# Kernel optimization log

Hardware: AMD Instinct MI355X
Metric: run time of the kernel (lower is better)

The kernel has to match this reference:

```python
import jax, jax.numpy as jnp
import numpy as np

DIM = 512
HEADS = 8
HEAD_DIM = DIM // HEADS
MLP_HIDDEN = int(DIM * 4.0)
B, N = 4, 2048
LS_INIT = 1e-5
EPS = 1e-5


def _layernorm(x, w, b):
    mu = jnp.mean(x, axis=-1, keepdims=True)
    var = jnp.mean(jnp.square(x - mu), axis=-1, keepdims=True)
    return (x - mu) * jax.lax.rsqrt(var + EPS) * w + b


def setup_inputs() -> dict:
    key = jax.random.key(0)
    ks = jax.random.split(key, 12)
    s = 0.02
    return {
        "x": jax.random.normal(ks[0], (B, N, DIM), jnp.float32),
        "rel_pos_bias": jax.random.normal(ks[1], (HEADS, N, N), jnp.float32),
        "qkv_w": jax.random.normal(ks[2], (DIM, 3 * DIM), jnp.float32) * s,
        "qkv_b": jnp.zeros((3 * DIM,), jnp.float32),
        "out_w": jax.random.normal(ks[3], (DIM, DIM), jnp.float32) * s,
        "out_b": jnp.zeros((DIM,), jnp.float32),
        "ln1_w": jnp.ones((DIM,), jnp.float32),
        "ln1_b": jnp.zeros((DIM,), jnp.float32),
        "ln2_w": jnp.ones((DIM,), jnp.float32),
        "ln2_b": jnp.zeros((DIM,), jnp.float32),
        "ffn_w1": jax.random.normal(ks[4], (DIM, MLP_HIDDEN), jnp.float32) * s,
        "ffn_b1": jnp.zeros((MLP_HIDDEN,), jnp.float32),
        "ffn_w2": jax.random.normal(ks[5], (MLP_HIDDEN, DIM), jnp.float32) * s,
        "ffn_b2": jnp.zeros((DIM,), jnp.float32),
        "gamma1": jnp.full((DIM,), LS_INIT, jnp.float32),
        "gamma2": jnp.full((DIM,), LS_INIT, jnp.float32),
    }


def reference(x, rel_pos_bias, qkv_w, qkv_b, out_w, out_b, ln1_w, ln1_b,
              ln2_w, ln2_b, ffn_w1, ffn_b1, ffn_w2, ffn_b2, gamma1, gamma2):
    # Pre-norm MHA with relative-position bias
    y = _layernorm(x, ln1_w, ln1_b)                       # [B,N,C]
    qkv = y @ qkv_w + qkv_b                               # [B,N,3C]
    qkv = qkv.reshape(B, N, 3, HEADS, HEAD_DIM)
    q = jnp.transpose(qkv[:, :, 0], (0, 2, 1, 3))         # [B,H,N,D]
    k = jnp.transpose(qkv[:, :, 1], (0, 2, 1, 3))
    v = jnp.transpose(qkv[:, :, 2], (0, 2, 1, 3))
    scale = 1.0 / np.sqrt(HEAD_DIM).astype(np.float32)
    attn = jnp.einsum("bhid,bhjd->bhij", q, k) * scale    # [B,H,N,N]
    attn = attn + rel_pos_bias[None]
    attn = jax.nn.softmax(attn, axis=-1)
    out = jnp.einsum("bhij,bhjd->bhid", attn, v)          # [B,H,N,D]
    out = jnp.transpose(out, (0, 2, 1, 3)).reshape(B, N, DIM)
    out = out @ out_w + out_b
    x = x + out * gamma1                                  # layer scale, no drop-path (eval)
    # FFN with exact GELU
    y2 = _layernorm(x, ln2_w, ln2_b)
    h = jax.nn.gelu(y2 @ ffn_w1 + ffn_b1, approximate=False)
    ffn_out = h @ ffn_w2 + ffn_b2
    x = x + ffn_out * gamma2
    return x
```

## Files before the change

kernel.cpp:

```cpp
#include <hip/hip_runtime.h>
#include <hip/hip_bf16.h>
#include <math.h>

#define SEQ 2048
#define BATCH 4
#define DM 512
#define NH 8
#define HD 64
#define HID 2048
#define ROWS (BATCH * SEQ)

typedef __attribute__((ext_vector_type(8))) short short8;
typedef __attribute__((ext_vector_type(4))) float f32x4;

__device__ __forceinline__ short f2bf(float f) {
    unsigned u = __float_as_uint(f);
    u += 0x7fff + ((u >> 16) & 1);
    return (short)(u >> 16);
}

__device__ __forceinline__ void gl2lds16(const void* g, void* l) {
    __builtin_amdgcn_global_load_lds(
        (const __attribute__((address_space(1))) void*)g,
        (__attribute__((address_space(3))) void*)l, 16, 0, 0);
}

__global__ __launch_bounds__(256) void tcast_all(
    const float* __restrict__ qkv_w, const float* __restrict__ out_w,
    const float* __restrict__ w1, const float* __restrict__ w2,
    short* __restrict__ o_qkv, short* __restrict__ o_out,
    short* __restrict__ o_w1, short* __restrict__ o_w2) {
    __shared__ float tile[32][33];
    int id = blockIdx.x;
    const float* W; short* O; int K, N;
    if (id < 768)       { W = qkv_w; O = o_qkv; K = 512;  N = 1536; }
    else if (id < 1024) { W = out_w; O = o_out; K = 512;  N = 512;  id -= 768; }
    else if (id < 2048) { W = w1;    O = o_w1;  K = 512;  N = 2048; id -= 1024; }
    else                { W = w2;    O = o_w2;  K = 2048; N = 512;  id -= 2048; }
    int tn = N / 32;
    int n0 = (id % tn) * 32, k0 = (id / tn) * 32;
    int tx = threadIdx.x, ty = threadIdx.y;
#pragma unroll
    for (int i = 0; i < 4; ++i)
        tile[ty + i * 8][tx] = W[(size_t)(k0 + ty + i * 8) * N + n0 + tx];
    __syncthreads();
#pragma unroll
    for (int i = 0; i < 4; ++i)
        O[(size_t)(n0 + ty + i * 8) * K + k0 + tx] = f2bf(tile[tx][ty + i * 8]);
}

__global__ __launch_bounds__(256) void ln_k(const float* __restrict__ X,
                                            const float* __restrict__ g,
                                            const float* __restrict__ bta,
                                            short* __restrict__ Y) {
    int t = threadIdx.x;
    int wv = t >> 6, ln = t & 63;
    size_t row = (size_t)blockIdx.x * 4 + wv;
    const float* xr = X + row * DM;
    float4 v0 = *(const float4*)(xr + ln * 4);
    float4 v1 = *(const float4*)(xr + 256 + ln * 4);
    float s = v0.x + v0.y + v0.z + v0.w + v1.x + v1.y + v1.z + v1.w;
    float q = v0.x * v0.x + v0.y * v0.y + v0.z * v0.z + v0.w * v0.w +
              v1.x * v1.x + v1.y * v1.y + v1.z * v1.z + v1.w * v1.w;
#pragma unroll
    for (int off = 1; off < 64; off <<= 1) {
        s += __shfl_xor(s, off);
        q += __shfl_xor(q, off);
    }
    float mean = s * (1.0f / 512.0f);
    float var = q * (1.0f / 512.0f) - mean * mean;
    float rstd = rsqrtf(var + 1e-5f);
    int c0 = ln * 4, c1 = 256 + ln * 4;
    ushort4 o0, o1;
    o0.x = (unsigned short)f2bf((v0.x - mean) * rstd * g[c0 + 0] + bta[c0 + 0]);
    o0.y = (unsigned short)f2bf((v0.y - mean) * rstd * g[c0 + 1] + bta[c0 + 1]);
    o0.z = (unsigned short)f2bf((v0.z - mean) * rstd * g[c0 + 2] + bta[c0 + 2]);
    o0.w = (unsigned short)f2bf((v0.w - mean) * rstd * g[c0 + 3] + bta[c0 + 3]);
    o1.x = (unsigned short)f2bf((v1.x - mean) * rstd * g[c1 + 0] + bta[c1 + 0]);
    o1.y = (unsigned short)f2bf((v1.y - mean) * rstd * g[c1 + 1] + bta[c1 + 1]);
    o1.z = (unsigned short)f2bf((v1.z - mean) * rstd * g[c1 + 2] + bta[c1 + 2]);
    o1.w = (unsigned short)f2bf((v1.w - mean) * rstd * g[c1 + 3] + bta[c1 + 3]);
    *(ushort4*)((unsigned short*)Y + row * DM + c0) = o0;
    *(ushort4*)((unsigned short*)Y + row * DM + c1) = o1;
}

template <int EPI, int TN, int BM>
__global__ __launch_bounds__(256) void gemm_bt(const short* __restrict__ A,
                                               const short* __restrict__ Bt,
                                               const float* __restrict__ bias,
                                               const float* __restrict__ gamma,
                                               const float* __restrict__ res,
                                               void* __restrict__ Cout,
                                               int M, int N, int K, int gx) {
    constexpr int NI = TN / 32;
    constexpr int MI = BM / 32;
    __shared__ __attribute__((aligned(16))) short As[2][2][BM][32];
    __shared__ __attribute__((aligned(16))) short Bs[2][2][TN][32];
    int t = threadIdx.x;
    int w = t >> 6, ln = t & 63;
    int quad = ln >> 4, l15 = ln & 15;
    int nwg = gridDim.x;
    int qq = nwg >> 3;
    int sw = ((blockIdx.x & 7) * qq) + (blockIdx.x >> 3);
    int bx = sw % gx, by = sw / gx;
    int n0 = bx * TN, m0 = by * BM;
    int wm = (w & 1) * (BM / 2), wn = (w >> 1) * (TN / 2);

    int srow0 = w * 32 + (ln >> 2);
    int srow1 = srow0 + 16;
    int srowH = w * 16 + (ln >> 2);
    int schunk = (ln & 3) * 8;
    const short* Ag0 = A + (size_t)(m0 + srow0) * K + schunk;
    const short* Ag1 = A + (size_t)(m0 + srow1) * K + schunk;
    const short* AgH = A + (size_t)(m0 + srowH) * K + schunk;
    const short* Bg0 = Bt + (size_t)(n0 + srow0) * K + schunk;
    const short* Bg1 = Bt + (size_t)(n0 + srow1) * K + schunk;
    const short* BgH = Bt + (size_t)(n0 + srowH) * K + schunk;

    f32x4 acc[MI][NI];
#pragma unroll
    for (int i = 0; i < MI; ++i)
#pragma unroll
        for (int j = 0; j < NI; ++j) acc[i][j] = (f32x4){0.f, 0.f, 0.f, 0.f};

    auto STAGE = [&](int buf, int k0) {
        if constexpr (BM == 128) {
            gl2lds16(Ag0 + k0, &As[buf][0][srow0][schunk]);
            gl2lds16(Ag1 + k0, &As[buf][0][srow1][schunk]);
            gl2lds16(Ag0 + k0 + 32, &As[buf][1][srow0][schunk]);
            gl2lds16(Ag1 + k0 + 32, &As[buf][1][srow1][schunk]);
        } else {
            gl2lds16(AgH + k0, &As[buf][0][srowH][schunk]);
            gl2lds16(AgH + k0 + 32, &As[buf][1][srowH][schunk]);
        }
        if constexpr (TN == 128) {
            gl2lds16(Bg0 + k0, &Bs[buf][0][srow0 & 127][schunk]);
            gl2lds16(Bg1 + k0, &Bs[buf][0][srow1 & 127][schunk]);
            gl2lds16(Bg0 + k0 + 32, &Bs[buf][1][srow0 & 127][schunk]);
            gl2lds16(Bg1 + k0 + 32, &Bs[buf][1][srow1 & 127][schunk]);
        } else {
            gl2lds16(BgH + k0, &Bs[buf][0][srowH & (TN - 1)][schunk]);
            gl2lds16(BgH + k0 + 32, &Bs[buf][1][srowH & (TN - 1)][schunk]);
        }
    };

    STAGE(0, 0);
    __syncthreads();

    int NS = K >> 6;
    for (int s = 0; s < NS; ++s) {
        int cur = s & 1;
        if (s + 1 < NS) STAGE(cur ^ 1, (s + 1) << 6);
#pragma unroll
        for (int hh = 0; hh < 2; ++hh) {
            short8 af[MI], bf[NI];
#pragma unroll
            for (int mi = 0; mi < MI; ++mi)
                af[mi] = *(const short8*)&As[cur][hh][wm + mi * 16 + l15][quad * 8];
#pragma unroll
            for (int ni = 0; ni < NI; ++ni)
                bf[ni] = *(const short8*)&Bs[cur][hh][wn + ni * 16 + l15][quad * 8];
#pragma unroll
            for (int mi = 0; mi < MI; ++mi)
#pragma unroll
                for (int ni = 0; ni < NI; ++ni)
                    acc[mi][ni] = __builtin_amdgcn_mfma_f32_16x16x32_bf16(
                        af[mi], bf[ni], acc[mi][ni], 0, 0, 0);
        }
        __syncthreads();
    }

#pragma unroll
    for (int mi = 0; mi < MI; ++mi) {
#pragma unroll
        for (int ni = 0; ni < NI; ++ni) {
#pragma unroll
            for (int r = 0; r < 4; ++r) {
                int row = m0 + wm + mi * 16 + quad * 4 + r;
                int col = n0 + wn + ni * 16 + l15;
                float v = acc[mi][ni][r] + bias[col];
                if (EPI == 0) {
                    ((short*)Cout)[(size_t)row * N + col] = f2bf(v);
                } else if (EPI == 1) {
                    float u = v * fmaf(v * v, 0.0713548162f, 1.59576912f);
                    float gg = v / (1.0f + __expf(-u));
                    ((short*)Cout)[(size_t)row * N + col] = f2bf(gg);
                } else {
                    ((float*)Cout)[(size_t)row * N + col] =
                        fmaf(v, gamma[col], res[(size_t)row * N + col]);
                }
            }
        }
    }
}

__global__ __launch_bounds__(256) void qkvbias_k(
    const short* __restrict__ A, const short* __restrict__ Bt,
    const float* __restrict__ qkvb, short* __restrict__ Cout,
    short* __restrict__ Cout2,
    const float* __restrict__ bias, short* __restrict__ biasP) {
    __shared__ __attribute__((aligned(16))) char smem[33024];
    int bid = blockIdx.x;
    int grp = bid / 11, sub = bid % 11;
    int t = threadIdx.x;
    int w = t >> 6, ln = t & 63;
    int quad = ln >> 4, l15 = ln & 15;

    if (sub < 3) {
        typedef short (*tile32)[32];
        tile32 As0 = (tile32)smem;
        tile32 As1 = (tile32)(smem + 8192);
        tile32 Bs0 = (tile32)(smem + 16384);
        tile32 Bs1 = (tile32)(smem + 24576);
        const int K = 512, N = 1536;
        int g = grp * 3 + sub;
        int n0 = (g % 12) * 128, m0 = (g / 12) * 128;
        int wm = (w & 1) * 64, wn = (w >> 1) * 64;

        int srow0 = w * 32 + (ln >> 2);
        int srow1 = srow0 + 16;
        int schunk = (ln & 3) * 8;
        const short* Ag0 = A + (size_t)(m0 + srow0) * K + schunk;
        const short* Ag1 = A + (size_t)(m0 + srow1) * K + schunk;
        const short* Bg0 = Bt + (size_t)(n0 + srow0) * K + schunk;
        const short* Bg1 = Bt + (size_t)(n0 + srow1) * K + schunk;

        f32x4 acc[4][4];
#pragma unroll
        for (int i = 0; i < 4; ++i)
#pragma unroll
            for (int j = 0; j < 4; ++j) acc[i][j] = (f32x4){0.f, 0.f, 0.f, 0.f};

        for (int k0 = 0; k0 < K; k0 += 64) {
            __syncthreads();
            gl2lds16(Ag0 + k0, &As0[srow0][schunk]);
            gl2lds16(Ag1 + k0, &As0[srow1][schunk]);
            gl2lds16(Ag0 + k0 + 32, &As1[srow0][schunk]);
            gl2lds16(Ag1 + k0 + 32, &As1[srow1][schunk]);
            gl2lds16(Bg0 + k0, &Bs0[srow0][schunk]);
            gl2lds16(Bg1 + k0, &Bs0[srow1][schunk]);
            gl2lds16(Bg0 + k0 + 32, &Bs1[srow0][schunk]);
            gl2lds16(Bg1 + k0 + 32, &Bs1[srow1][schunk]);
            __syncthreads();
            {
                short8 af[4], bf[4];
#pragma unroll
                for (int mi = 0; mi < 4; ++mi)
                    af[mi] = *(const short8*)&As0[wm + mi * 16 + l15][quad * 8];
#pragma unroll
                for (int ni = 0; ni < 4; ++ni)
                    bf[ni] = *(const short8*)&Bs0[wn + ni * 16 + l15][quad * 8];
#pragma unroll
                for (int mi = 0; mi < 4; ++mi)
#pragma unroll
                    for (int ni = 0; ni < 4; ++ni)
                        acc[mi][ni] = __builtin_amdgcn_mfma_f32_16x16x32_bf16(
                            af[mi], bf[ni], acc[mi][ni], 0, 0, 0);
            }
            {
                short8 af[4], bf[4];
#pragma unroll
                for (int mi = 0; mi < 4; ++mi)
                    af[mi] = *(const short8*)&As1[wm + mi * 16 + l15][quad * 8];
#pragma unroll
                for (int ni = 0; ni < 4; ++ni)
                    bf[ni] = *(const short8*)&Bs1[wn + ni * 16 + l15][quad * 8];
#pragma unroll
                for (int mi = 0; mi < 4; ++mi)
#pragma unroll
                    for (int ni = 0; ni < 4; ++ni)
                        acc[mi][ni] = __builtin_amdgcn_mfma_f32_16x16x32_bf16(
                            af[mi], bf[ni], acc[mi][ni], 0, 0, 0);
            }
        }

        if (n0 >= 1024) {
#pragma unroll
            for (int mi = 0; mi < 4; ++mi) {
#pragma unroll
                for (int ni = 0; ni < 4; ++ni) {
                    int col = n0 + wn + ni * 16 + l15;
                    int d = col - 1024, hh = d >> 6, dd = d & 63;
                    int row0 = m0 + wm + mi * 16 + quad * 4;
                    int bb = row0 >> 11, key = row0 & 2047;
                    float bs = qkvb[col];
                    ushort4 pk;
                    pk.x = (unsigned short)f2bf(acc[mi][ni][0] + bs);
                    pk.y = (unsigned short)f2bf(acc[mi][ni][1] + bs);
                    pk.z = (unsigned short)f2bf(acc[mi][ni][2] + bs);
                    pk.w = (unsigned short)f2bf(acc[mi][ni][3] + bs);
                    *(ushort4*)&Cout2[((size_t)(bb * 8 + hh) * 64 + dd) * 2048 + key] = pk;
                }
            }
        } else {
#pragma unroll
            for (int mi = 0; mi < 4; ++mi) {
#pragma unroll
                for (int ni = 0; ni < 4; ++ni) {
#pragma unroll
                    for (int r = 0; r < 4; ++r) {
                        int row = m0 + wm + mi * 16 + quad * 4 + r;
                        int col = n0 + wn + ni * 16 + l15;
                        float v = acc[mi][ni][r] + qkvb[col];
                        float sc = (n0 < 512) ? 0.18033688f : 1.0f;
                        Cout[(size_t)row * 1024 + col] = f2bf(v * sc);
                    }
                }
            }
        }
    } else {
        typedef short (*tile1032)[1032];
        tile1032 tl = (tile1032)smem;
        int id = grp * 8 + (sub - 3);
        int half = id & 1;
        int g = (id >> 1) & 127;
        int h = id >> 8;
        const float* src = bias + (size_t)h * SEQ * SEQ + (size_t)g * 16 * SEQ + half * 1024;
#pragma unroll
        for (int i = 0; i < 16; ++i) {
            float4 v = *(const float4*)(src + (size_t)i * SEQ + t * 4);
            float2 lo, hi;
            lo.x = v.x * 1.44269504f; lo.y = v.y * 1.44269504f;
            hi.x = v.z * 1.44269504f; hi.y = v.w * 1.44269504f;
            __hip_bfloat162 l2 = __float22bfloat162_rn(lo);
            __hip_bfloat162 h2 = __float22bfloat162_rn(hi);
            uint2 pp;
            pp.x = *(unsigned*)&l2;
            pp.y = *(unsigned*)&h2;
            *(uint2*)&tl[i][t * 4] = pp;
        }
        __syncthreads();
        int jtbase = half * 16;
#pragma unroll
        for (int u = 0; u < 4; ++u) {
            int jl = w * 4 + u;
            int tau = (h * 128 + g) * 32 + jtbase + jl;
#pragma unroll
            for (int n2 = 0; n2 < 2; ++n2) {
                uint2 a = *(const uint2*)&tl[l15][jl * 64 + n2 * 32 + quad * 4];
                uint2 b = *(const uint2*)&tl[l15][jl * 64 + n2 * 32 + 16 + quad * 4];
                uint4 pp;
                pp.x = a.x; pp.y = a.y; pp.z = b.x; pp.w = b.y;
                *(uint4*)(biasP + (size_t)tau * 1024 + n2 * 512 + ln * 8) = pp;
            }
        }
    }
}

__global__ __launch_bounds__(256, 3) void attn_k(const short* __restrict__ qkv,
                                                 const short* __restrict__ vT,
                                                 const short* __restrict__ biasP,
                                                 short* __restrict__ Aout) {
    __shared__ __attribute__((aligned(16))) short Ks[2][64 * 64];
    __shared__ __attribute__((aligned(16))) short Vs[2][64 * 64];
    __shared__ __attribute__((aligned(16))) short Ps[4][2][16 * 64];
    int t = threadIdx.x;
    int w = t >> 6, ln = t & 63, quad = ln >> 4, l15 = ln & 15;
    int idx = blockIdx.x;
    int h = idx & 7, b = (idx >> 3) & 3, qt = idx >> 5;
    int qb = qt * 128 + w * 16;
    const size_t cbase = (size_t)b * SEQ * 1024;

    const short* qrow0 = qkv + cbase + (size_t)(qb + l15) * 1024 + h * 64;
    const short* qrow1 = qrow0 + (size_t)64 * 1024;
    short8 qf[2][2];
    qf[0][0] = *(const short8*)(qrow0 + quad * 8);
    qf[0][1] = *(const short8*)(qrow0 + 32 + quad * 8);
    qf[1][0] = *(const short8*)(qrow1 + quad * 8);
    qf[1][1] = *(const short8*)(qrow1 + 32 + quad * 8);

    int kr = t >> 3, kc = t & 7;
    int sc = (kc ^ (kr & 7)) * 8;
    const short* kgS = qkv + cbase + 512 + h * 64 + sc;
    const short* vgS = vT + (size_t)(b * 8 + h) * 64 * 2048 + sc;

    int g0 = qt * 8 + w;
    const short* bp0 = biasP + ((size_t)(h * 128 + g0) * 32) * 1024 + ln * 8;
    const short* bp1 = biasP + ((size_t)(h * 128 + g0 + 4) * 32) * 1024 + ln * 8;

    short8 ones;
#pragma unroll
    for (int i = 0; i < 8; ++i) ones[i] = (short)0x3F80;

    f32x4 o[2][4], ol[2];
#pragma unroll
    for (int qg = 0; qg < 2; ++qg) {
#pragma unroll
        for (int db = 0; db < 4; ++db) o[qg][db] = (f32x4){0.f, 0.f, 0.f, 0.f};
        ol[qg] = (f32x4){0.f, 0.f, 0.f, 0.f};
    }

    int sw7 = l15 & 7;

    gl2lds16(kgS,                              &Ks[0][t * 8]);
    gl2lds16(kgS + (size_t)32 * 1024,          &Ks[0][2048 + t * 8]);
    gl2lds16(vgS,                              &Vs[0][t * 8]);
    gl2lds16(vgS + (size_t)32 * 2048,          &Vs[0][2048 + t * 8]);
    uint4 bbc[2][2];
#pragma unroll
    for (int n2 = 0; n2 < 2; ++n2) {
        bbc[0][n2] = *(const uint4*)(bp0 + n2 * 512);
        bbc[1][n2] = *(const uint4*)(bp1 + n2 * 512);
    }

    int cur = 0;
    for (int jt = 0; jt < 32; ++jt) {
        __syncthreads();
        int jn = (jt < 31) ? (jt + 1) : jt;
        int j1 = jn * 64;
        int nxt = cur ^ 1;
        gl2lds16(kgS + (size_t)(j1 + kr) * 1024,      &Ks[nxt][t * 8]);
        gl2lds16(kgS + (size_t)(j1 + 32 + kr) * 1024, &Ks[nxt][2048 + t * 8]);
        gl2lds16(vgS + (size_t)kr * 2048 + j1,        &Vs[nxt][t * 8]);
        gl2lds16(vgS + (size_t)(32 + kr) * 2048 + j1, &Vs[nxt][2048 + t * 8]);

        f32x4 s4[2][4];
#pragma unroll
        for (int ni = 0; ni < 4; ++ni) {
            short8 k0 = *(const short8*)&Ks[cur][(ni * 16 + l15) * 64 + ((quad ^ sw7) * 8)];
            short8 k1 = *(const short8*)&Ks[cur][(ni * 16 + l15) * 64 + (((4 + quad) ^ sw7) * 8)];
#pragma unroll
            for (int qg = 0; qg < 2; ++qg) {
                uint4 bb = bbc[qg][ni >> 1];
                unsigned lo = (ni & 1) ? bb.z : bb.x;
                unsigned hi = (ni & 1) ? bb.w : bb.y;
                f32x4 z;
                z[0] = __uint_as_float(lo << 16);
                z[1] = __uint_as_float(lo & 0xffff0000u);
                z[2] = __uint_as_float(hi << 16);
                z[3] = __uint_as_float(hi & 0xffff0000u);
                z = __builtin_amdgcn_mfma_f32_16x16x32_bf16(k0, qf[qg][0], z, 0, 0, 0);
                s4[qg][ni] = __builtin_amdgcn_mfma_f32_16x16x32_bf16(k1, qf[qg][1], z, 0, 0, 0);
            }
        }
#pragma unroll
        for (int n2 = 0; n2 < 2; ++n2) {
            bbc[0][n2] = *(const uint4*)(bp0 + (size_t)jn * 1024 + n2 * 512);
            bbc[1][n2] = *(const uint4*)(bp1 + (size_t)jn * 1024 + n2 * 512);
        }
#pragma unroll
        for (int qg = 0; qg < 2; ++qg) {
#pragma unroll
            for (int ni = 0; ni < 4; ++ni) {
                float2 plo, phi;
                plo.x = exp2f(s4[qg][ni][0]);
                plo.y = exp2f(s4[qg][ni][1]);
                phi.x = exp2f(s4[qg][ni][2]);
                phi.y = exp2f(s4[qg][ni][3]);
                __hip_bfloat162 l2 = __float22bfloat162_rn(plo);
                __hip_bfloat162 h2 = __float22bfloat162_rn(phi);
                union { uint2 u; } pp;
                pp.u.x = *(unsigned*)&l2;
                pp.u.y = *(unsigned*)&h2;
                int c = ni * 2 + (quad >> 1);
                *(uint2*)&Ps[w][qg][l15 * 64 + ((c ^ sw7) * 8) + (quad & 1) * 4] = pp.u;
            }
        }
#pragma unroll
        for (int kk = 0; kk < 2; ++kk) {
            short8 ap0 = *(const short8*)&Ps[w][0][l15 * 64 + (((kk * 4 + quad) ^ sw7) * 8)];
            short8 ap1 = *(const short8*)&Ps[w][1][l15 * 64 + (((kk * 4 + quad) ^ sw7) * 8)];
#pragma unroll
            for (int db = 0; db < 4; ++db) {
                short8 vv = *(const short8*)&Vs[cur][(db * 16 + l15) * 64 + (((kk * 4 + quad) ^ sw7) * 8)];
                o[0][db] = __builtin_amdgcn_mfma_f32_16x16x32_bf16(ap0, vv, o[0][db], 0, 0, 0);
                o[1][db] = __builtin_amdgcn_mfma_f32_16x16x32_bf16(ap1, vv, o[1][db], 0, 0, 0);
            }
            ol[0] = __builtin_amdgcn_mfma_f32_16x16x32_bf16(ap0, ones, ol[0], 0, 0, 0);
            ol[1] = __builtin_amdgcn_mfma_f32_16x16x32_bf16(ap1, ones, ol[1], 0, 0, 0);
        }
        cur = nxt;
    }
#pragma unroll
    for (int qg = 0; qg < 2; ++qg) {
#pragma unroll
        for (int r = 0; r < 4; ++r) {
            float inv = 1.0f / ol[qg][r];
            int qrow_g = b * SEQ + qb + qg * 64 + quad * 4 + r;
#pragma unroll
            for (int db = 0; db < 4; ++db) {
                Aout[(size_t)qrow_g * DM + h * 64 + db * 16 + l15] =
                    f2bf(o[qg][db][r] * inv);
            }
        }
    }
}

extern "C" void kernel_launch(void* const* d_in, const int* in_sizes, int n_in,
                              void* d_out, int out_size, void* d_ws, size_t ws_size,
                              hipStream_t stream) {
    const float* x      = (const float*)d_in[0];
    const float* bias   = (const float*)d_in[1];
    const float* qkv_w  = (const float*)d_in[2];
    const float* qkv_b  = (const float*)d_in[3];
    const float* out_w  = (const float*)d_in[4];
    const float* out_b  = (const float*)d_in[5];
    const float* ln1_w  = (const float*)d_in[6];
    const float* ln1_b  = (const float*)d_in[7];
    const float* ln2_w  = (const float*)d_in[8];
    const float* ln2_b  = (const float*)d_in[9];
    const float* ffn_w1 = (const float*)d_in[10];
    const float* ffn_b1 = (const float*)d_in[11];
    const float* ffn_w2 = (const float*)d_in[12];
    const float* ffn_b2 = (const float*)d_in[13];
    const float* gamma1 = (const float*)d_in[14];
    const float* gamma2 = (const float*)d_in[15];
    float* out = (float*)d_out;

    short* wqkvT = (short*)d_ws;
    short* woutT = wqkvT + (size_t)1536 * 512;
    short* w1T   = woutT + (size_t)512 * 512;
    short* w2T   = w1T + (size_t)2048 * 512;
    short* y1    = w2T + (size_t)512 * 2048;
    short* qkvB  = y1 + (size_t)ROWS * DM;
    short* vTb   = qkvB + (size_t)ROWS * 1024;
    short* aoutB = vTb + (size_t)32 * 64 * 2048;
    float* x1    = (float*)(aoutB + (size_t)ROWS * DM);
    short* biasPw = (short*)(x1 + (size_t)ROWS * DM);
    short* hB    = qkvB;

    tcast_all<<<3072, dim3(32, 8), 0, stream>>>(qkv_w, out_w, ffn_w1, ffn_w2,
                                                wqkvT, woutT, w1T, w2T);
    ln_k<<<ROWS / 4, 256, 0, stream>>>(x, ln1_w, ln1_b, y1);
    qkvbias_k<<<2816, 256, 0, stream>>>(y1, wqkvT, qkv_b, qkvB, vTb,
                                        bias, biasPw);
    attn_k<<<512, 256, 0, stream>>>(qkvB, vTb, biasPw, aoutB);
    gemm_bt<2, 128, 64><<<512, 256, 0, stream>>>(
        aoutB, woutT, out_b, gamma1, x, x1, ROWS, 512, 512, 4);
    ln_k<<<ROWS / 4, 256, 0, stream>>>(x1, ln2_w, ln2_b, y1);
    gemm_bt<1, 128, 128><<<1024, 256, 0, stream>>>(
        y1, w1T, ffn_b1, nullptr, nullptr, hB, ROWS, 2048, 512, 16);
    gemm_bt<2, 128, 64><<<512, 256, 0, stream>>>(
        hB, w2T, ffn_b2, gamma2, x1, out, ROWS, 512, 2048, 4);
}
```

Baseline: 420.7 us.

## Merge weight cast, LN1 and bias repack into one prep kernel; standalone QKV GEMM

Weight transpose-cast, the first layernorm and the rel-pos-bias repack now run as interleaved block roles inside a single prep kernel. The QKV GEMM moves out of the bias-repack kernel into the templated double-buffered gemm_bt with a new epilogue that scales q and writes V transposed. The aim is to overlap the memory-bound prep work across all CUs, cut one launch, and let the QKV GEMM use the pipelined GEMM path. In exchange, the QKV GEMM no longer overlaps with the bias repack.

```diff
diff --git a/kernel.cpp b/kernel.cpp
--- a/kernel.cpp
+++ b/kernel.cpp
@@ -25,28 +25,105 @@
         (__attribute__((address_space(3))) void*)l, 16, 0, 0);
 }
 
-__global__ __launch_bounds__(256) void tcast_all(
+__global__ __launch_bounds__(256) void prep_k(
     const float* __restrict__ qkv_w, const float* __restrict__ out_w,
     const float* __restrict__ w1, const float* __restrict__ w2,
     short* __restrict__ o_qkv, short* __restrict__ o_out,
-    short* __restrict__ o_w1, short* __restrict__ o_w2) {
-    __shared__ float tile[32][33];
-    int id = blockIdx.x;
-    const float* W; short* O; int K, N;
-    if (id < 768)       { W = qkv_w; O = o_qkv; K = 512;  N = 1536; }
-    else if (id < 1024) { W = out_w; O = o_out; K = 512;  N = 512;  id -= 768; }
-    else if (id < 2048) { W = w1;    O = o_w1;  K = 512;  N = 2048; id -= 1024; }
-    else                { W = w2;    O = o_w2;  K = 2048; N = 512;  id -= 2048; }
-    int tn = N / 32;
-    int n0 = (id % tn) * 32, k0 = (id / tn) * 32;
-    int tx = threadIdx.x, ty = threadIdx.y;
-#pragma unroll
-    for (int i = 0; i < 4; ++i)
-        tile[ty + i * 8][tx] = W[(size_t)(k0 + ty + i * 8) * N + n0 + tx];
-    __syncthreads();
-#pragma unroll
-    for (int i = 0; i < 4; ++i)
-        O[(size_t)(n0 + ty + i * 8) * K + k0 + tx] = f2bf(tile[tx][ty + i * 8]);
+    short* __restrict__ o_w1, short* __restrict__ o_w2,
+    const float* __restrict__ X, const float* __restrict__ lg,
+    const float* __restrict__ lb, short* __restrict__ Y,
+    const float* __restrict__ bias, short* __restrict__ biasP) {
+    __shared__ __attribute__((aligned(16))) char smem[33024];
+    int bid = blockIdx.x;
+    int grp = bid / 7, sub = bid % 7;
+    int t = threadIdx.x;
+
+    if (sub < 3) {
+        float (*tile)[33] = (float(*)[33])smem;
+        int id = grp * 3 + sub;
+        const float* W; short* O; int K, N;
+        if (id < 768)       { W = qkv_w; O = o_qkv; K = 512;  N = 1536; }
+        else if (id < 1024) { W = out_w; O = o_out; K = 512;  N = 512;  id -= 768; }
+        else if (id < 2048) { W = w1;    O = o_w1;  K = 512;  N = 2048; id -= 1024; }
+        else                { W = w2;    O = o_w2;  K = 2048; N = 512;  id -= 2048; }
+        int tn = N / 32;
+        int n0 = (id % tn) * 32, k0 = (id / tn) * 32;
+        int tx = t & 31, ty = t >> 5;
+#pragma unroll
+        for (int i = 0; i < 4; ++i)
+            tile[ty + i * 8][tx] = W[(size_t)(k0 + ty + i * 8) * N + n0 + tx];
+        __syncthreads();
+#pragma unroll
+        for (int i = 0; i < 4; ++i)
+            O[(size_t)(n0 + ty + i * 8) * K + k0 + tx] = f2bf(tile[tx][ty + i * 8]);
+    } else if (sub < 5) {
+        int lbk = grp * 2 + (sub - 3);
+        int wv = t >> 6, ln = t & 63;
+        size_t row = (size_t)lbk * 4 + wv;
+        const float* xr = X + row * DM;
+        float4 v0 = *(const float4*)(xr + ln * 4);
+        float4 v1 = *(const float4*)(xr + 256 + ln * 4);
+        float s = v0.x + v0.y + v0.z + v0.w + v1.x + v1.y + v1.z + v1.w;
+        float q = v0.x * v0.x + v0.y * v0.y + v0.z * v0.z + v0.w * v0.w +
+                  v1.x * v1.x + v1.y * v1.y + v1.z * v1.z + v1.w * v1.w;
+#pragma unroll
+        for (int off = 1; off < 64; off <<= 1) {
+            s += __shfl_xor(s, off);
+            q += __shfl_xor(q, off);
+        }
+        float mean = s * (1.0f / 512.0f);
+        float var = q * (1.0f / 512.0f) - mean * mean;
+        float rstd = rsqrtf(var + 1e-5f);
+        int c0 = ln * 4, c1 = 256 + ln * 4;
+        ushort4 o0, o1;
+        o0.x = (unsigned short)f2bf((v0.x - mean) * rstd * lg[c0 + 0] + lb[c0 + 0]);
+        o0.y = (unsigned short)f2bf((v0.y - mean) * rstd * lg[c0 + 1] + lb[c0 + 1]);
+        o0.z = (unsigned short)f2bf((v0.z - mean) * rstd * lg[c0 + 2] + lb[c0 + 2]);
+        o0.w = (unsigned short)f2bf((v0.w - mean) * rstd * lg[c0 + 3] + lb[c0 + 3]);
+        o1.x = (unsigned short)f2bf((v1.x - mean) * rstd * lg[c1 + 0] + lb[c1 + 0]);
+        o1.y = (unsigned short)f2bf((v1.y - mean) * rstd * lg[c1 + 1] + lb[c1 + 1]);
+        o1.z = (unsigned short)f2bf((v1.z - mean) * rstd * lg[c1 + 2] + lb[c1 + 2]);
+        o1.w = (unsigned short)f2bf((v1.w - mean) * rstd * lg[c1 + 3] + lb[c1 + 3]);
+        *(ushort4*)((unsigned short*)Y + row * DM + c0) = o0;
+        *(ushort4*)((unsigned short*)Y + row * DM + c1) = o1;
+    } else {
+        typedef short (*tile1032)[1032];
+        tile1032 tl = (tile1032)smem;
+        int id = grp * 2 + (sub - 5);
+        int w = t >> 6, ln = t & 63, quad = ln >> 4, l15 = ln & 15;
+        int half = id & 1;
+        int g = (id >> 1) & 127;
+        int h = id >> 8;
+        const float* src = bias + (size_t)h * SEQ * SEQ + (size_t)g * 16 * SEQ + half * 1024;
+#pragma unroll
+        for (int i = 0; i < 16; ++i) {
+            float4 v = *(const float4*)(src + (size_t)i * SEQ + t * 4);
+            float2 lo, hi;
+            lo.x = v.x * 1.44269504f; lo.y = v.y * 1.44269504f;
+            hi.x = v.z * 1.44269504f; hi.y = v.w * 1.44269504f;
+            __hip_bfloat162 l2 = __float22bfloat162_rn(lo);
+            __hip_bfloat162 h2 = __float22bfloat162_rn(hi);
+            uint2 pp;
+            pp.x = *(unsigned*)&l2;
+            pp.y = *(unsigned*)&h2;
+            *(uint2*)&tl[i][t * 4] = pp;
+        }
+        __syncthreads();
+        int jtbase = half * 16;
+#pragma unroll
+        for (int u = 0; u < 4; ++u) {
+            int jl = w * 4 + u;
+            int tau = (h * 128 + g) * 32 + jtbase + jl;
+#pragma unroll
+            for (int n2 = 0; n2 < 2; ++n2) {
+                uint2 a = *(const uint2*)&tl[l15][jl * 64 + n2 * 32 + quad * 4];
+                uint2 b = *(const uint2*)&tl[l15][jl * 64 + n2 * 32 + 16 + quad * 4];
+                uint4 pp;
+                pp.x = a.x; pp.y = a.y; pp.z = b.x; pp.w = b.y;
+                *(uint4*)(biasP + (size_t)tau * 1024 + n2 * 512 + ln * 8) = pp;
+            }
+        }
+    }
 }
 
 __global__ __launch_bounds__(256) void ln_k(const float* __restrict__ X,
@@ -91,6 +168,7 @@
                                                const float* __restrict__ gamma,
                                                const float* __restrict__ res,
                                                void* __restrict__ Cout,
+                                               short* __restrict__ Cout2,
                                                int M, int N, int K, int gx) {
     constexpr int NI = TN / 32;
     constexpr int MI = BM / 32;
@@ -170,178 +248,48 @@
         __syncthreads();
     }
 
-#pragma unroll
-    for (int mi = 0; mi < MI; ++mi) {
-#pragma unroll
-        for (int ni = 0; ni < NI; ++ni) {
-#pragma unroll
-            for (int r = 0; r < 4; ++r) {
-                int row = m0 + wm + mi * 16 + quad * 4 + r;
+    if (EPI == 3 && n0 >= 1024) {
+#pragma unroll
+        for (int mi = 0; mi < MI; ++mi) {
+#pragma unroll
+            for (int ni = 0; ni < NI; ++ni) {
                 int col = n0 + wn + ni * 16 + l15;
-                float v = acc[mi][ni][r] + bias[col];
-                if (EPI == 0) {
-                    ((short*)Cout)[(size_t)row * N + col] = f2bf(v);
-                } else if (EPI == 1) {
-                    float u = v * fmaf(v * v, 0.0713548162f, 1.59576912f);
-                    float gg = v / (1.0f + __expf(-u));
-                    ((short*)Cout)[(size_t)row * N + col] = f2bf(gg);
-                } else {
-                    ((float*)Cout)[(size_t)row * N + col] =
-                        fmaf(v, gamma[col], res[(size_t)row * N + col]);
-                }
-            }
-        }
-    }
-}
-
-__global__ __launch_bounds__(256) void qkvbias_k(
-    const short* __restrict__ A, const short* __restrict__ Bt,
-    const float* __restrict__ qkvb, short* __restrict__ Cout,
-    short* __restrict__ Cout2,
-    const float* __restrict__ bias, short* __restrict__ biasP) {
-    __shared__ __attribute__((aligned(16))) char smem[33024];
-    int bid = blockIdx.x;
-    int grp = bid / 11, sub = bid % 11;
-    int t = threadIdx.x;
-    int w = t >> 6, ln = t & 63;
-    int quad = ln >> 4, l15 = ln & 15;
-
-    if (sub < 3) {
-        typedef short (*tile32)[32];
-        tile32 As0 = (tile32)smem;
-        tile32 As1 = (tile32)(smem + 8192);
-        tile32 Bs0 = (tile32)(smem + 16384);
-        tile32 Bs1 = (tile32)(smem + 24576);
-        const int K = 512, N = 1536;
-        int g = grp * 3 + sub;
-        int n0 = (g % 12) * 128, m0 = (g / 12) * 128;
-        int wm = (w & 1) * 64, wn = (w >> 1) * 64;
-
-        int srow0 = w * 32 + (ln >> 2);
-        int srow1 = srow0 + 16;
-        int schunk = (ln & 3) * 8;
-        const short* Ag0 = A + (size_t)(m0 + srow0) * K + schunk;
-        const short* Ag1 = A + (size_t)(m0 + srow1) * K + schunk;
-        const short* Bg0 = Bt + (size_t)(n0 + srow0) * K + schunk;
-        const short* Bg1 = Bt + (size_t)(n0 + srow1) * K + schunk;
-
-        f32x4 acc[4][4];
-#pragma unroll
-        for (int i = 0; i < 4; ++i)
-#pragma unroll
-            for (int j = 0; j < 4; ++j) acc[i][j] = (f32x4){0.f, 0.f, 0.f, 0.f};
-
-        for (int k0 = 0; k0 < K; k0 += 64) {
-            __syncthreads();
-            gl2lds16(Ag0 + k0, &As0[srow0][schunk]);
-            gl2lds16(Ag1 + k0, &As0[srow1][schunk]);
-            gl2lds16(Ag0 + k0 + 32, &As1[srow0][schunk]);
-            gl2lds16(Ag1 + k0 + 32, &As1[srow1][schunk]);
-            gl2lds16(Bg0 + k0, &Bs0[srow0][schunk]);
-            gl2lds16(Bg1 + k0, &Bs0[srow1][schunk]);
-            gl2lds16(Bg0 + k0 + 32, &Bs1[srow0][schunk]);
-            gl2lds16(Bg1 + k0 + 32, &Bs1[srow1][schunk]);
-            __syncthreads();
-            {
-                short8 af[4], bf[4];
-#pragma unroll
-                for (int mi = 0; mi < 4; ++mi)
-                    af[mi] = *(const short8*)&As0[wm + mi * 16 + l15][quad * 8];
-#pragma unroll
-                for (int ni = 0; ni < 4; ++ni)
-                    bf[ni] = *(const short8*)&Bs0[wn + ni * 16 + l15][quad * 8];
-#pragma unroll
-                for (int mi = 0; mi < 4; ++mi)
-#pragma unroll
-                    for (int ni = 0; ni < 4; ++ni)
-                        acc[mi][ni] = __builtin_amdgcn_mfma_f32_16x16x32_bf16(
-                            af[mi], bf[ni], acc[mi][ni], 0, 0, 0);
-            }
-            {
-                short8 af[4], bf[4];
-#pragma unroll
-                for (int mi = 0; mi < 4; ++mi)
-                    af[mi] = *(const short8*)&As1[wm + mi * 16 + l15][quad * 8];
-#pragma unroll
-                for (int ni = 0; ni < 4; ++ni)
-                    bf[ni] = *(const short8*)&Bs1[wn + ni * 16 + l15][quad * 8];
-#pragma unroll
-                for (int mi = 0; mi < 4; ++mi)
-#pragma unroll
-                    for (int ni = 0; ni < 4; ++ni)
-                        acc[mi][ni] = __builtin_amdgcn_mfma_f32_16x16x32_bf16(
-                            af[mi], bf[ni], acc[mi][ni], 0, 0, 0);
-            }
-        }
-
-        if (n0 >= 1024) {
-#pragma unroll
-            for (int mi = 0; mi < 4; ++mi) {
-#pragma unroll
-                for (int ni = 0; ni < 4; ++ni) {
+                int d = col - 1024, hh2 = d >> 6, dd = d & 63;
+                int row0 = m0 + wm + mi * 16 + quad * 4;
+                int bb = row0 >> 11, key = row0 & 2047;
+                float bs = bias[col];
+                ushort4 pk;
+                pk.x = (unsigned short)f2bf(acc[mi][ni][0] + bs);
+                pk.y = (unsigned short)f2bf(acc[mi][ni][1] + bs);
+                pk.z = (unsigned short)f2bf(acc[mi][ni][2] + bs);
+                pk.w = (unsigned short)f2bf(acc[mi][ni][3] + bs);
+                *(ushort4*)&Cout2[((size_t)(bb * 8 + hh2) * 64 + dd) * 2048 + key] = pk;
+            }
+        }
+    } else {
+#pragma unroll
+        for (int mi = 0; mi < MI; ++mi) {
+#pragma unroll
+            for (int ni = 0; ni < NI; ++ni) {
+#pragma unroll
+                for (int r = 0; r < 4; ++r) {
+                    int row = m0 + wm + mi * 16 + quad * 4 + r;
                     int col = n0 + wn + ni * 16 + l15;
-                    int d = col - 1024, hh = d >> 6, dd = d & 63;
-                    int row0 = m0 + wm + mi * 16 + quad * 4;
-                    int bb = row0 >> 11, key = row0 & 2047;
-                    float bs = qkvb[col];
-                    ushort4 pk;
-                    pk.x = (unsigned short)f2bf(acc[mi][ni][0] + bs);
-                    pk.y = (unsigned short)f2bf(acc[mi][ni][1] + bs);
-                    pk.z = (unsigned short)f2bf(acc[mi][ni][2] + bs);
-                    pk.w = (unsigned short)f2bf(acc[mi][ni][3] + bs);
-                    *(ushort4*)&Cout2[((size_t)(bb * 8 + hh) * 64 + dd) * 2048 + key] = pk;
-                }
-            }
-        } else {
-#pragma unroll
-            for (int mi = 0; mi < 4; ++mi) {
-#pragma unroll
-                for (int ni = 0; ni < 4; ++ni) {
-#pragma unroll
-                    for (int r = 0; r < 4; ++r) {
-                        int row = m0 + wm + mi * 16 + quad * 4 + r;
-                        int col = n0 + wn + ni * 16 + l15;
-                        float v = acc[mi][ni][r] + qkvb[col];
+                    float v = acc[mi][ni][r] + bias[col];
+                    if (EPI == 0) {
+                        ((short*)Cout)[(size_t)row * N + col] = f2bf(v);
+                    } else if (EPI == 1) {
+                        float u = v * fmaf(v * v, 0.0713548162f, 1.59576912f);
+                        float gg = v / (1.0f + __expf(-u));
+                        ((short*)Cout)[(size_t)row * N + col] = f2bf(gg);
+                    } else if (EPI == 2) {
+                        ((float*)Cout)[(size_t)row * N + col] =
+                            fmaf(v, gamma[col], res[(size_t)row * N + col]);
+                    } else {
                         float sc = (n0 < 512) ? 0.18033688f : 1.0f;
-                        Cout[(size_t)row * 1024 + col] = f2bf(v * sc);
+                        ((short*)Cout)[(size_t)row * 1024 + col] = f2bf(v * sc);
                     }
                 }
-            }
-        }
-    } else {
-        typedef short (*tile1032)[1032];
-        tile1032 tl = (tile1032)smem;
-        int id = grp * 8 + (sub - 3);
-        int half = id & 1;
-        int g = (id >> 1) & 127;
-        int h = id >> 8;
-        const float* src = bias + (size_t)h * SEQ * SEQ + (size_t)g * 16 * SEQ + half * 1024;
-#pragma unroll
-        for (int i = 0; i < 16; ++i) {
-            float4 v = *(const float4*)(src + (size_t)i * SEQ + t * 4);
-            float2 lo, hi;
-            lo.x = v.x * 1.44269504f; lo.y = v.y * 1.44269504f;
-            hi.x = v.z * 1.44269504f; hi.y = v.w * 1.44269504f;
-            __hip_bfloat162 l2 = __float22bfloat162_rn(lo);
-            __hip_bfloat162 h2 = __float22bfloat162_rn(hi);
-            uint2 pp;
-            pp.x = *(unsigned*)&l2;
-            pp.y = *(unsigned*)&h2;
-            *(uint2*)&tl[i][t * 4] = pp;
-        }
-        __syncthreads();
-        int jtbase = half * 16;
-#pragma unroll
-        for (int u = 0; u < 4; ++u) {
-            int jl = w * 4 + u;
-            int tau = (h * 128 + g) * 32 + jtbase + jl;
-#pragma unroll
-            for (int n2 = 0; n2 < 2; ++n2) {
-                uint2 a = *(const uint2*)&tl[l15][jl * 64 + n2 * 32 + quad * 4];
-                uint2 b = *(const uint2*)&tl[l15][jl * 64 + n2 * 32 + 16 + quad * 4];
-                uint4 pp;
-                pp.x = a.x; pp.y = a.y; pp.z = b.x; pp.w = b.y;
-                *(uint4*)(biasP + (size_t)tau * 1024 + n2 * 512 + ln * 8) = pp;
             }
         }
     }
@@ -519,17 +467,18 @@
     short* biasPw = (short*)(x1 + (size_t)ROWS * DM);
     short* hB    = qkvB;
 
-    tcast_all<<<3072, dim3(32, 8), 0, stream>>>(qkv_w, out_w, ffn_w1, ffn_w2,
-                                                wqkvT, woutT, w1T, w2T);
-    ln_k<<<ROWS / 4, 256, 0, stream>>>(x, ln1_w, ln1_b, y1);
-    qkvbias_k<<<2816, 256, 0, stream>>>(y1, wqkvT, qkv_b, qkvB, vTb,
-                                        bias, biasPw);
+    prep_k<<<7168, 256, 0, stream>>>(qkv_w, out_w, ffn_w1, ffn_w2,
+                                     wqkvT, woutT, w1T, w2T,
+                                     x, ln1_w, ln1_b, y1,
+                                     bias, biasPw);
+    gemm_bt<3, 128, 128><<<768, 256, 0, stream>>>(
+        y1, wqkvT, qkv_b, nullptr, nullptr, qkvB, vTb, ROWS, 1536, 512, 12);
     attn_k<<<512, 256, 0, stream>>>(qkvB, vTb, biasPw, aoutB);
     gemm_bt<2, 128, 64><<<512, 256, 0, stream>>>(
-        aoutB, woutT, out_b, gamma1, x, x1, ROWS, 512, 512, 4);
+        aoutB, woutT, out_b, gamma1, x, x1, nullptr, ROWS, 512, 512, 4);
     ln_k<<<ROWS / 4, 256, 0, stream>>>(x1, ln2_w, ln2_b, y1);
     gemm_bt<1, 128, 128><<<1024, 256, 0, stream>>>(
-        y1, w1T, ffn_b1, nullptr, nullptr, hB, ROWS, 2048, 512, 16);
+        y1, w1T, ffn_b1, nullptr, nullptr, hB, nullptr, ROWS, 2048, 512, 16);
     gemm_bt<2, 128, 64><<<512, 256, 0, stream>>>(
-        hB, w2T, ffn_b2, gamma2, x1, out, ROWS, 512, 2048, 4);
-}
+        hB, w2T, ffn_b2, gamma2, x1, out, nullptr, ROWS, 512, 2048, 4);
+}
```

After: 427.7 us. About the same (+1.7%).
